# Kernel optimization log

Hardware: AMD Instinct MI355X
Metric: run time of the kernel (lower is better)

## Reference

```python
import jax, jax.numpy as jnp
import numpy as np

BATCH_SIZE = 4096
NUM_CAMS = 64
D_FEAT = 512
EPS = 1e-16  # standard safe-sqrt epsilon used by utils.euclidean_distance_matrix


def setup_inputs() -> dict:
    key = jax.random.key(0)
    x = jax.random.normal(key, (BATCH_SIZE, D_FEAT), dtype=jnp.float32)
    # calc_idx: row i indexes the (frprcam-1) same-camera off-diagonal slots,
    # all rows in a block share idx = arange(frprcam-1) + block_start
    frprcam = BATCH_SIZE // NUM_CAMS
    uf = frprcam - 1
    block_start = (np.arange(BATCH_SIZE) // frprcam) * frprcam
    idxs = jnp.asarray(block_start[:, None] + np.arange(uf)[None, :], dtype=jnp.int32)
    return {"x": x, "idxs": idxs}


def _euclidean_distance_matrix(x):
    # ||xi - xj||: gram trick with zero-masking so sqrt is safe at 0
    dot = x @ x.T                                  # [B,B]
    sq = jnp.diagonal(dot)                         # [B]
    d2 = jax.nn.relu(sq[:, None] - 2.0 * dot + sq[None, :])
    zero = (d2 == 0.0).astype(x.dtype)
    return jnp.sqrt(d2 + zero * EPS) * (1.0 - zero)


def reference(x, idxs):
    bs = x.shape[0]
    dist = _euclidean_distance_matrix(x)           # [B,B]
    # drop the diagonal: flatten()[1:].view(B-1, B+1)[:, :-1] trick
    offdiag = dist.reshape(-1)[1:].reshape(bs - 1, bs + 1)[:, :-1].reshape(bs, bs - 1)
    logits = jax.nn.softmax(-offdiag, axis=1)      # [B,B-1]
    p = jnp.take_along_axis(logits, idxs, axis=1).sum(axis=1)  # [B]
    return (-jnp.log(p)).sum() / bs
```

## Files before the change

### kernel.cpp

```cpp
#include <hip/hip_runtime.h>
#include <hip/hip_bf16.h>

#define BATCH 4096
#define DFEAT 512
#define TM 128
#define TN 128
#define BK 64
#define NB (BATCH / TM)
#define NPAIR (NB * (NB + 1) / 2)
#define NXCD 8
#define CPX (NPAIR / NXCD)

typedef __attribute__((ext_vector_type(8))) __bf16 bf16x8;
typedef __attribute__((ext_vector_type(4))) float f32x4;

__device__ inline ushort f2bf(float f) {
    uint u = __float_as_uint(f);
    uint r = (u + 0x7FFFu + ((u >> 16) & 1u)) >> 16;
    return (ushort)r;
}

__global__ __launch_bounds__(256) void prep_kernel(
        const float* __restrict__ x, ushort* __restrict__ xb,
        float* __restrict__ sqx, float* __restrict__ num, float* __restrict__ den,
        float* __restrict__ out) {
    int t = blockIdx.x * 256 + threadIdx.x;
    if (t < BATCH) { num[t] = 0.0f; den[t] = 0.0f; }
    if (t == 0) out[0] = 0.0f;
    int wid = threadIdx.x >> 6, lane = threadIdx.x & 63;
    int row = blockIdx.x * 4 + wid;
    const float* xr = x + (size_t)row * DFEAT + lane * 8;
    float4 v0 = *(const float4*)(xr);
    float4 v1 = *(const float4*)(xr + 4);
    float f[8] = {v0.x, v0.y, v0.z, v0.w, v1.x, v1.y, v1.z, v1.w};
    float s = 0.0f;
#pragma unroll
    for (int i = 0; i < 8; i++) s += f[i] * f[i];
    uint us[4];
#pragma unroll
    for (int i = 0; i < 4; i++)
        us[i] = (uint)f2bf(f[2 * i]) | ((uint)f2bf(f[2 * i + 1]) << 16);
    *(uint4*)&xb[(size_t)row * DFEAT + lane * 8] = *(uint4*)us;
#pragma unroll
    for (int m = 32; m; m >>= 1) s += __shfl_xor(s, m, 64);
    if (lane == 0) sqx[row] = s;
}

__global__ __launch_bounds__(256) void dist_kernel(
        const ushort* __restrict__ xb, const float* __restrict__ sqx,
        float* __restrict__ num, float* __restrict__ den) {
    __shared__ __align__(16) ushort As[2][TM * BK];
    __shared__ __align__(16) ushort Bs[2][TN * BK];

    int bid = blockIdx.x;
    int idx = (bid % NXCD) * CPX + bid / NXCD;

    float nb5 = (float)NB + 0.5f;
    int rb = (int)(nb5 - sqrtf(nb5 * nb5 - 2.0f * (float)idx));
    while (rb > 0 && rb * NB - rb * (rb - 1) / 2 > idx) rb--;
    while ((rb + 1) * NB - (rb + 1) * rb / 2 <= idx) rb++;
    int cb = rb + idx - (rb * NB - rb * (rb - 1) / 2);

    const int rowbase = rb * TM, colbase = cb * TN;
    const int tid = threadIdx.x;
    const int wid = tid >> 6, lane = tid & 63;
    const int wr = wid >> 1, wc = wid & 1;
    const int l15 = lane & 15, l4 = lane >> 4;

    f32x4 acc[4][4] = {};

    auto stage = [&](int buf, int kb) {
#pragma unroll
        for (int q = 0; q < 4; q++) {
            int u = q * 256 + tid;
            int r = u >> 3;
            int cch = ((u & 7) ^ (r & 7)) << 3;
            const ushort* ga = &xb[(size_t)(rowbase + r) * DFEAT + kb + cch];
            const ushort* gb = &xb[(size_t)(colbase + r) * DFEAT + kb + cch];
            ushort* la = &As[buf][(q * 256 + wid * 64) * 8];
            ushort* lb = &Bs[buf][(q * 256 + wid * 64) * 8];
            __builtin_amdgcn_global_load_lds(
                (const __attribute__((address_space(1))) void*)ga,
                (__attribute__((address_space(3))) void*)la, 16, 0, 0);
            __builtin_amdgcn_global_load_lds(
                (const __attribute__((address_space(1))) void*)gb,
                (__attribute__((address_space(3))) void*)lb, 16, 0, 0);
        }
    };

    auto compute = [&](int buf) {
#pragma unroll
        for (int kk = 0; kk < BK; kk += 32) {
            bf16x8 a[4], b[4];
#pragma unroll
            for (int mi = 0; mi < 4; mi++) {
                int ra = wr * 64 + mi * 16 + l15;
                a[mi] = *(const bf16x8*)
                    &As[buf][ra * BK + ((((kk >> 3) + l4) ^ (ra & 7)) << 3)];
            }
#pragma unroll
            for (int ni = 0; ni < 4; ni++) {
                int rc = wc * 64 + ni * 16 + l15;
                b[ni] = *(const bf16x8*)
                    &Bs[buf][rc * BK + ((((kk >> 3) + l4) ^ (rc & 7)) << 3)];
            }
#pragma unroll
            for (int mi = 0; mi < 4; mi++)
#pragma unroll
                for (int ni = 0; ni < 4; ni++)
                    acc[mi][ni] = __builtin_amdgcn_mfma_f32_16x16x32_bf16(
                        a[mi], b[ni], acc[mi][ni], 0, 0, 0);
        }
    };

    stage(0, 0);
    __syncthreads();
    int cur = 0;
#pragma unroll 1
    for (int t = 0; t < DFEAT / BK - 1; t++) {
        stage(cur ^ 1, (t + 1) * BK);
        compute(cur);
        __syncthreads();
        cur ^= 1;
    }
    compute(cur);

    float sj[4];
#pragma unroll
    for (int ni = 0; ni < 4; ni++) sj[ni] = sqx[colbase + wc * 64 + ni * 16 + l15];

    if (rb == cb) {
#pragma unroll
        for (int mi = 0; mi < 4; mi++) {
#pragma unroll
            for (int r = 0; r < 4; r++) {
                const int i = rowbase + wr * 64 + mi * 16 + 4 * l4 + r;
                const float si = sqx[i];
                float np = 0.0f, dp = 0.0f;
#pragma unroll
                for (int ni = 0; ni < 4; ni++) {
                    const int j = colbase + wc * 64 + ni * 16 + l15;
                    float d2 = fmaxf(si + sj[ni] - 2.0f * acc[mi][ni][r], 0.0f);
                    float e = (i == j) ? 0.0f : __expf(-sqrtf(d2));
                    dp += e;
                    np += ((i >> 6) == (j >> 6)) ? e : 0.0f;
                }
#pragma unroll
                for (int m = 1; m <= 8; m <<= 1) {
                    np += __shfl_xor(np, m, 64);
                    dp += __shfl_xor(dp, m, 64);
                }
                if (l15 == 0) {
                    atomicAdd(&num[i], np);
                    atomicAdd(&den[i], dp);
                }
            }
        }
    } else {
        float cde[4] = {0.0f, 0.0f, 0.0f, 0.0f};
#pragma unroll
        for (int mi = 0; mi < 4; mi++) {
#pragma unroll
            for (int r = 0; r < 4; r++) {
                const int i = rowbase + wr * 64 + mi * 16 + 4 * l4 + r;
                const float si = sqx[i];
                float dp = 0.0f;
#pragma unroll
                for (int ni = 0; ni < 4; ni++) {
                    float d2 = fmaxf(si + sj[ni] - 2.0f * acc[mi][ni][r], 0.0f);
                    float e = __expf(-sqrtf(d2));
                    dp += e;
                    cde[ni] += e;
                }
#pragma unroll
                for (int m = 1; m <= 8; m <<= 1) dp += __shfl_xor(dp, m, 64);
                if (l15 == 0) atomicAdd(&den[i], dp);
            }
        }
#pragma unroll
        for (int ni = 0; ni < 4; ni++) {
            float c = cde[ni];
            c += __shfl_xor(c, 16, 64);
            c += __shfl_xor(c, 32, 64);
            if (l4 == 0) atomicAdd(&den[colbase + wc * 64 + ni * 16 + l15], c);
        }
    }
}

__global__ __launch_bounds__(256) void loss_kernel(
        const float* __restrict__ num, const float* __restrict__ den,
        float* __restrict__ out) {
    __shared__ float red[4];
    int t = blockIdx.x * 256 + threadIdx.x;
    float s = logf(den[t]) - logf(num[t]);
#pragma unroll
    for (int m = 32; m; m >>= 1) s += __shfl_xor(s, m, 64);
    int wid = threadIdx.x >> 6, lane = threadIdx.x & 63;
    if (lane == 0) red[wid] = s;
    __syncthreads();
    if (threadIdx.x == 0)
        atomicAdd(out, (red[0] + red[1] + red[2] + red[3]) * (1.0f / (float)BATCH));
}

extern "C" void kernel_launch(void* const* d_in, const int* in_sizes, int n_in,
                              void* d_out, int out_size, void* d_ws, size_t ws_size,
                              hipStream_t stream) {
    const float* x = (const float*)d_in[0];
    char* ws = (char*)d_ws;
    ushort* xb = (ushort*)ws;
    float* sqx = (float*)(ws + (size_t)BATCH * DFEAT * 2);
    float* num = sqx + BATCH;
    float* den = num + BATCH;
    float* out = (float*)d_out;

    prep_kernel<<<BATCH / 4, 256, 0, stream>>>(x, xb, sqx, num, den, out);
    dist_kernel<<<NPAIR, 256, 0, stream>>>(xb, sqx, num, den);
    loss_kernel<<<BATCH / 256, 256, 0, stream>>>(num, den, out);
}
```

Before: 102.7 us.

## Use 8-wave blocks, deeper async LDS prefetch, and per-tile partial-sum buffers

Doubles the workgroup to 512 threads (8 waves, each covering 64x32 of the 128x128 tile) and restructures the K loop to prefetch two stages ahead with explicit vmcnt waits and raw barriers. It also replaces the contended atomics on a single den array with per-block-pair partial arrays P and Q, which are zeroed in prep and summed in the loss kernel. The aim is to raise occupancy and latency hiding and to cut atomic contention, at the cost of a larger workspace, extra zeroing and a serial reduction loop in the loss kernel.

```diff
diff --git a/kernel.cpp b/kernel.cpp
--- a/kernel.cpp
+++ b/kernel.cpp
@@ -3,13 +3,13 @@
 
 #define BATCH 4096
 #define DFEAT 512
-#define TM 128
-#define TN 128
+#define TT 128
 #define BK 64
-#define NB (BATCH / TM)
-#define NPAIR (NB * (NB + 1) / 2)
+#define NBP (BATCH / TT)
+#define NPAIR (NBP * (NBP + 1) / 2)
 #define NXCD 8
 #define CPX (NPAIR / NXCD)
+#define ZCOUNT (2 * NBP * BATCH + BATCH)
 
 typedef __attribute__((ext_vector_type(8))) __bf16 bf16x8;
 typedef __attribute__((ext_vector_type(4))) float f32x4;
@@ -22,10 +22,10 @@
 
 __global__ __launch_bounds__(256) void prep_kernel(
         const float* __restrict__ x, ushort* __restrict__ xb,
-        float* __restrict__ sqx, float* __restrict__ num, float* __restrict__ den,
+        float* __restrict__ sqx, float* __restrict__ zbase,
         float* __restrict__ out) {
     int t = blockIdx.x * 256 + threadIdx.x;
-    if (t < BATCH) { num[t] = 0.0f; den[t] = 0.0f; }
+    for (int u = t; u < ZCOUNT; u += 256 * (BATCH / 4)) zbase[u] = 0.0f;
     if (t == 0) out[0] = 0.0f;
     int wid = threadIdx.x >> 6, lane = threadIdx.x & 63;
     int row = blockIdx.x * 4 + wid;
@@ -46,39 +46,39 @@
     if (lane == 0) sqx[row] = s;
 }
 
-__global__ __launch_bounds__(256) void dist_kernel(
+__global__ __launch_bounds__(512, 4) void dist_kernel(
         const ushort* __restrict__ xb, const float* __restrict__ sqx,
-        float* __restrict__ num, float* __restrict__ den) {
-    __shared__ __align__(16) ushort As[2][TM * BK];
-    __shared__ __align__(16) ushort Bs[2][TN * BK];
+        float* __restrict__ P, float* __restrict__ Q, float* __restrict__ numv) {
+    __shared__ __align__(16) ushort As[2][TT * BK];
+    __shared__ __align__(16) ushort Bs[2][TT * BK];
 
     int bid = blockIdx.x;
-    int idx = (bid % NXCD) * CPX + bid / NXCD;
-
-    float nb5 = (float)NB + 0.5f;
+    int idx = (bid & (NXCD - 1)) * CPX + (bid >> 3);
+
+    float nb5 = (float)NBP + 0.5f;
     int rb = (int)(nb5 - sqrtf(nb5 * nb5 - 2.0f * (float)idx));
-    while (rb > 0 && rb * NB - rb * (rb - 1) / 2 > idx) rb--;
-    while ((rb + 1) * NB - (rb + 1) * rb / 2 <= idx) rb++;
-    int cb = rb + idx - (rb * NB - rb * (rb - 1) / 2);
-
-    const int rowbase = rb * TM, colbase = cb * TN;
+    while (rb > 0 && rb * NBP - rb * (rb - 1) / 2 > idx) rb--;
+    while ((rb + 1) * NBP - (rb + 1) * rb / 2 <= idx) rb++;
+    int cb = rb + idx - (rb * NBP - rb * (rb - 1) / 2);
+
+    const int rowbase = rb * TT, colbase = cb * TT;
     const int tid = threadIdx.x;
     const int wid = tid >> 6, lane = tid & 63;
-    const int wr = wid >> 1, wc = wid & 1;
+    const int wr = wid >> 2, wc = wid & 3;
     const int l15 = lane & 15, l4 = lane >> 4;
 
-    f32x4 acc[4][4] = {};
+    f32x4 acc[4][2] = {};
 
     auto stage = [&](int buf, int kb) {
 #pragma unroll
-        for (int q = 0; q < 4; q++) {
-            int u = q * 256 + tid;
-            int r = u >> 3;
-            int cch = ((u & 7) ^ (r & 7)) << 3;
-            const ushort* ga = &xb[(size_t)(rowbase + r) * DFEAT + kb + cch];
-            const ushort* gb = &xb[(size_t)(colbase + r) * DFEAT + kb + cch];
-            ushort* la = &As[buf][(q * 256 + wid * 64) * 8];
-            ushort* lb = &Bs[buf][(q * 256 + wid * 64) * 8];
+        for (int q = 0; q < 2; q++) {
+            int e = q * 512 + tid;
+            int r = e >> 3;
+            int c8 = ((e & 7) ^ (r & 7)) << 3;
+            const ushort* ga = &xb[(size_t)(rowbase + r) * DFEAT + kb + c8];
+            const ushort* gb = &xb[(size_t)(colbase + r) * DFEAT + kb + c8];
+            ushort* la = &As[buf][(q * 512 + wid * 64) * 8];
+            ushort* lb = &Bs[buf][(q * 512 + wid * 64) * 8];
             __builtin_amdgcn_global_load_lds(
                 (const __attribute__((address_space(1))) void*)ga,
                 (__attribute__((address_space(3))) void*)la, 16, 0, 0);
@@ -91,7 +91,7 @@
     auto compute = [&](int buf) {
 #pragma unroll
         for (int kk = 0; kk < BK; kk += 32) {
-            bf16x8 a[4], b[4];
+            bf16x8 a[4], b[2];
 #pragma unroll
             for (int mi = 0; mi < 4; mi++) {
                 int ra = wr * 64 + mi * 16 + l15;
@@ -99,35 +99,43 @@
                     &As[buf][ra * BK + ((((kk >> 3) + l4) ^ (ra & 7)) << 3)];
             }
 #pragma unroll
-            for (int ni = 0; ni < 4; ni++) {
-                int rc = wc * 64 + ni * 16 + l15;
+            for (int ni = 0; ni < 2; ni++) {
+                int rc = wc * 32 + ni * 16 + l15;
                 b[ni] = *(const bf16x8*)
                     &Bs[buf][rc * BK + ((((kk >> 3) + l4) ^ (rc & 7)) << 3)];
             }
 #pragma unroll
             for (int mi = 0; mi < 4; mi++)
 #pragma unroll
-                for (int ni = 0; ni < 4; ni++)
+                for (int ni = 0; ni < 2; ni++)
                     acc[mi][ni] = __builtin_amdgcn_mfma_f32_16x16x32_bf16(
                         a[mi], b[ni], acc[mi][ni], 0, 0, 0);
         }
     };
 
     stage(0, 0);
-    __syncthreads();
-    int cur = 0;
-#pragma unroll 1
-    for (int t = 0; t < DFEAT / BK - 1; t++) {
-        stage(cur ^ 1, (t + 1) * BK);
-        compute(cur);
-        __syncthreads();
-        cur ^= 1;
+    stage(1, BK);
+#pragma unroll
+    for (int t = 0; t < DFEAT / BK; t++) {
+        if (t == DFEAT / BK - 1)
+            asm volatile("s_waitcnt vmcnt(0)" ::: "memory");
+        else
+            asm volatile("s_waitcnt vmcnt(4)" ::: "memory");
+        __builtin_amdgcn_sched_barrier(0);
+        __builtin_amdgcn_s_barrier();
+        __builtin_amdgcn_sched_barrier(0);
+        compute(t & 1);
+        if (t < DFEAT / BK - 2) {
+            __builtin_amdgcn_sched_barrier(0);
+            __builtin_amdgcn_s_barrier();
+            __builtin_amdgcn_sched_barrier(0);
+            stage(t & 1, (t + 2) * BK);
+        }
     }
-    compute(cur);
-
-    float sj[4];
-#pragma unroll
-    for (int ni = 0; ni < 4; ni++) sj[ni] = sqx[colbase + wc * 64 + ni * 16 + l15];
+
+    float sj[2];
+#pragma unroll
+    for (int ni = 0; ni < 2; ni++) sj[ni] = sqx[colbase + wc * 32 + ni * 16 + l15];
 
     if (rb == cb) {
 #pragma unroll
@@ -136,10 +144,10 @@
             for (int r = 0; r < 4; r++) {
                 const int i = rowbase + wr * 64 + mi * 16 + 4 * l4 + r;
                 const float si = sqx[i];
-                float np = 0.0f, dp = 0.0f;
-#pragma unroll
-                for (int ni = 0; ni < 4; ni++) {
-                    const int j = colbase + wc * 64 + ni * 16 + l15;
+                float dp = 0.0f, np = 0.0f;
+#pragma unroll
+                for (int ni = 0; ni < 2; ni++) {
+                    const int j = colbase + wc * 32 + ni * 16 + l15;
                     float d2 = fmaxf(si + sj[ni] - 2.0f * acc[mi][ni][r], 0.0f);
                     float e = (i == j) ? 0.0f : __expf(-sqrtf(d2));
                     dp += e;
@@ -147,17 +155,17 @@
                 }
 #pragma unroll
                 for (int m = 1; m <= 8; m <<= 1) {
+                    dp += __shfl_xor(dp, m, 64);
                     np += __shfl_xor(np, m, 64);
-                    dp += __shfl_xor(dp, m, 64);
                 }
                 if (l15 == 0) {
-                    atomicAdd(&num[i], np);
-                    atomicAdd(&den[i], dp);
+                    atomicAdd(&P[(size_t)cb * BATCH + i], dp);
+                    if (np != 0.0f) atomicAdd(&numv[i], np);
                 }
             }
         }
     } else {
-        float cde[4] = {0.0f, 0.0f, 0.0f, 0.0f};
+        float cde[2] = {0.0f, 0.0f};
 #pragma unroll
         for (int mi = 0; mi < 4; mi++) {
 #pragma unroll
@@ -166,7 +174,7 @@
                 const float si = sqx[i];
                 float dp = 0.0f;
 #pragma unroll
-                for (int ni = 0; ni < 4; ni++) {
+                for (int ni = 0; ni < 2; ni++) {
                     float d2 = fmaxf(si + sj[ni] - 2.0f * acc[mi][ni][r], 0.0f);
                     float e = __expf(-sqrtf(d2));
                     dp += e;
@@ -174,25 +182,30 @@
                 }
 #pragma unroll
                 for (int m = 1; m <= 8; m <<= 1) dp += __shfl_xor(dp, m, 64);
-                if (l15 == 0) atomicAdd(&den[i], dp);
-            }
-        }
-#pragma unroll
-        for (int ni = 0; ni < 4; ni++) {
+                if (l15 == 0) atomicAdd(&P[(size_t)cb * BATCH + i], dp);
+            }
+        }
+#pragma unroll
+        for (int ni = 0; ni < 2; ni++) {
             float c = cde[ni];
             c += __shfl_xor(c, 16, 64);
             c += __shfl_xor(c, 32, 64);
-            if (l4 == 0) atomicAdd(&den[colbase + wc * 64 + ni * 16 + l15], c);
+            if (l4 == 0)
+                atomicAdd(&Q[(size_t)rb * BATCH + colbase + wc * 32 + ni * 16 + l15], c);
         }
     }
 }
 
 __global__ __launch_bounds__(256) void loss_kernel(
-        const float* __restrict__ num, const float* __restrict__ den,
-        float* __restrict__ out) {
+        const float* __restrict__ P, const float* __restrict__ Q,
+        const float* __restrict__ numv, float* __restrict__ out) {
     __shared__ float red[4];
-    int t = blockIdx.x * 256 + threadIdx.x;
-    float s = logf(den[t]) - logf(num[t]);
+    const int i = blockIdx.x * 256 + threadIdx.x;
+    const int p = i >> 7;
+    float den = 0.0f;
+    for (int cb = p; cb < NBP; cb++) den += P[(size_t)cb * BATCH + i];
+    for (int rb = 0; rb < p; rb++) den += Q[(size_t)rb * BATCH + i];
+    float s = logf(den) - logf(numv[i]);
 #pragma unroll
     for (int m = 32; m; m >>= 1) s += __shfl_xor(s, m, 64);
     int wid = threadIdx.x >> 6, lane = threadIdx.x & 63;
@@ -209,11 +222,12 @@
     char* ws = (char*)d_ws;
     ushort* xb = (ushort*)ws;
     float* sqx = (float*)(ws + (size_t)BATCH * DFEAT * 2);
-    float* num = sqx + BATCH;
-    float* den = num + BATCH;
+    float* P = sqx + BATCH;
+    float* Q = P + (size_t)NBP * BATCH;
+    float* numv = Q + (size_t)NBP * BATCH;
     float* out = (float*)d_out;
 
-    prep_kernel<<<BATCH / 4, 256, 0, stream>>>(x, xb, sqx, num, den, out);
-    dist_kernel<<<NPAIR, 256, 0, stream>>>(xb, sqx, num, den);
-    loss_kernel<<<BATCH / 256, 256, 0, stream>>>(num, den, out);
-}
+    prep_kernel<<<BATCH / 4, 256, 0, stream>>>(x, xb, sqx, P, out);
+    dist_kernel<<<NPAIR, 512, 0, stream>>>(xb, sqx, P, Q, numv);
+    loss_kernel<<<BATCH / 256, 256, 0, stream>>>(P, Q, numv, out);
+}
```

After: 103.1 us. No clear change (+0.4%).
